# Kernel tuning notes

Measured on AMD Instinct MI355X. Metric: run time of the kernel, lower is better.

The kernel has to match this reference:

```python
import jax, jax.numpy as jnp
import numpy as np

NQ = 4            # num_qubits
DIM = 2 ** NQ     # 16-dim complex state

def _rx(theta):
    c = jnp.cos(theta / 2.0); s = jnp.sin(theta / 2.0)
    return jnp.array([[c, -1j * s], [-1j * s, c]], dtype=jnp.complex64)

def _ry(theta):
    c = jnp.cos(theta / 2.0); s = jnp.sin(theta / 2.0)
    return jnp.array([[c, -s], [s, c]], dtype=jnp.complex64)

def _apply_1q(state, q, U):
    # state: [B, 16] complex; apply 2x2 unitary U on qubit q (qubit 0 = MSB)
    B = state.shape[0]
    st = state.reshape((B,) + (2,) * NQ)
    st = jnp.moveaxis(st, 1 + q, -1)
    st = st @ U.T
    st = jnp.moveaxis(st, -1, 1 + q)
    return st.reshape(B, DIM)

def _apply_cnot(state, c, t):
    # flip target qubit t where control qubit c == 1
    B = state.shape[0]
    st = state.reshape((B,) + (2,) * NQ)
    st = jnp.moveaxis(st, (1 + c, 1 + t), (-2, -1))
    st = jnp.stack([st[..., 0, :], st[..., 1, ::-1]], axis=-2)
    st = jnp.moveaxis(st, (-2, -1), (1 + c, 1 + t))
    return st.reshape(B, DIM)

def _circuit(state):
    rx1, ry1 = _rx(0.1), _ry(0.2)
    rx2, ry2 = _rx(0.3), _ry(0.4)
    for q in range(NQ):
        state = _apply_1q(state, q, rx1)
        state = _apply_1q(state, q, ry1)
    for q in range(NQ - 1):
        state = _apply_cnot(state, q, q + 1)
    for q in range(NQ):
        state = _apply_1q(state, q, rx2)
        state = _apply_1q(state, q, ry2)
    return state

def setup_inputs() -> dict:
    key = jax.random.key(0)
    ks = jax.random.split(key, 9)
    B = 65536
    return {
        'x':   jax.random.normal(ks[0], (B, 784), dtype=jnp.float32),
        'We1': jax.random.normal(ks[1], (784, 256), dtype=jnp.float32) * 0.05,
        'be1': jnp.zeros((256,), dtype=jnp.float32),
        'We2': jax.random.normal(ks[2], (256, 32), dtype=jnp.float32) * 0.05,
        'be2': jnp.zeros((32,), dtype=jnp.float32),
        'W1':  jax.random.normal(ks[3], (32, 128), dtype=jnp.float32) * 0.05,
        'b1':  jnp.zeros((128,), dtype=jnp.float32),
        'W2':  jax.random.normal(ks[4], (128, 10), dtype=jnp.float32) * 0.05,
        'b2':  jnp.zeros((10,), dtype=jnp.float32),
    }

def reference(x, We1, be1, We2, be2, W1, b1, W2, b2):
    # encoder: Linear(784,256) -> ReLU -> Linear(256,32) -> Tanh
    h = jax.nn.relu(x @ We1 + be1)
    enc = jnp.tanh(h @ We2 + be2)               # [B, 32]
    psi = (enc[:, :DIM] + 1j * enc[:, DIM:]).astype(jnp.complex64)
    norm = jnp.sqrt(jnp.sum(jnp.abs(psi) ** 2, axis=1, keepdims=True))
    psi = psi / norm
    psi = _circuit(psi)                          # [B, 16] complex
    feat = jnp.concatenate([psi.real, psi.imag], axis=1)  # [B, 32]
    # classifier: Linear(32,128) -> ReLU -> (Dropout=identity in eval) -> Linear(128,10)
    out = jax.nn.relu(feat @ W1 + b1) @ W2 + b2
    return out
```

## Files before the change

### kernel.cpp

```cpp
#include <hip/hip_runtime.h>
#include <stdint.h>

#define DEVINL __device__ __forceinline__

typedef short bf16x8 __attribute__((ext_vector_type(8)));
typedef float f32x4  __attribute__((ext_vector_type(4)));

DEVINL uint16_t f2bf(float f) {
    uint32_t u = __builtin_bit_cast(uint32_t, f);
    uint32_t r = u + 0x7fffu + ((u >> 16) & 1u);
    return (uint16_t)(r >> 16);
}

DEVINL f32x4 mfma16x16x32(bf16x8 a, bf16x8 b, f32x4 c) {
    return __builtin_amdgcn_mfma_f32_16x16x32_bf16(a, b, c, 0, 0, 0);
}

DEVINL void async_load16(const void* g, void* l) {
    __builtin_amdgcn_global_load_lds(
        (const __attribute__((address_space(1))) void*)g,
        (__attribute__((address_space(3))) void*)l, 16, 0, 0);
}

#define WS_WE1T 0
#define WS_WE2T 425984
#define WS_W1T  442368
#define WS_W2T  450560

__global__ __launch_bounds__(256) void prep_weights(
    const float* __restrict__ We1, const float* __restrict__ We2,
    const float* __restrict__ W1,  const float* __restrict__ W2,
    uint16_t* __restrict__ We1T, uint16_t* __restrict__ We2T,
    uint16_t* __restrict__ W1T,  uint16_t* __restrict__ W2T) {
    int tid = blockIdx.x * 256 + threadIdx.x;
    if (tid < 256 * 832) {
        int n = tid / 832, k = tid % 832;
        We1T[tid] = (k < 784) ? f2bf(We1[k * 256 + n]) : (uint16_t)0;
        return;
    }
    int t2 = tid - 256 * 832;
    if (t2 < 32 * 256) {
        int n = t2 / 256, k = t2 % 256;
        We2T[t2] = f2bf(We2[k * 32 + n]);
        return;
    }
    int t3 = t2 - 32 * 256;
    if (t3 < 128 * 32) {
        int n = t3 / 32, k = t3 % 32;
        W1T[t3] = f2bf(W1[k * 128 + n]);
        return;
    }
    int t4 = t3 - 128 * 32;
    if (t4 < 16 * 128) {
        int n = t4 / 128, k = t4 % 128;
        W2T[t4] = (n < 10) ? f2bf(W2[k * 10 + n]) : (uint16_t)0;
        return;
    }
}

DEVINL void apply_rx(float* sr, float* si, int bit, float c, float s) {
    #pragma unroll
    for (int i = 0; i < 16; i++) {
        if (!(i & bit)) {
            int j = i | bit;
            float r0 = sr[i], i0 = si[i], r1 = sr[j], i1 = si[j];
            sr[i] = c * r0 + s * i1;  si[i] = c * i0 - s * r1;
            sr[j] = c * r1 + s * i0;  si[j] = c * i1 - s * r0;
        }
    }
}
DEVINL void apply_ry(float* sr, float* si, int bit, float c, float s) {
    #pragma unroll
    for (int i = 0; i < 16; i++) {
        if (!(i & bit)) {
            int j = i | bit;
            float r0 = sr[i], i0 = si[i], r1 = sr[j], i1 = si[j];
            sr[i] = c * r0 - s * r1;  si[i] = c * i0 - s * i1;
            sr[j] = s * r0 + c * r1;  si[j] = s * i0 + c * i1;
        }
    }
}
DEVINL void apply_cnot(float* sr, float* si, int cb, int tb) {
    #pragma unroll
    for (int i = 0; i < 16; i++) {
        if ((i & cb) && !(i & tb)) {
            int j = i | tb;
            float tr = sr[i]; sr[i] = sr[j]; sr[j] = tr;
            float ti = si[i]; si[i] = si[j]; si[j] = ti;
        }
    }
}
DEVINL void circuit(float* sr, float* si) {
    const float C1 = 0.99875026039496628f, S1 = 0.04997916927067833f;
    const float C2 = 0.99500416527802582f, S2 = 0.09983341664682815f;
    const float C3 = 0.98877107793604227f, S3 = 0.14943813247359922f;
    const float C4 = 0.98006657784124163f, S4 = 0.19866933079506122f;
    #pragma unroll
    for (int q = 0; q < 4; q++) {
        int bit = 8 >> q;
        apply_rx(sr, si, bit, C1, S1);
        apply_ry(sr, si, bit, C2, S2);
    }
    apply_cnot(sr, si, 8, 4);
    apply_cnot(sr, si, 4, 2);
    apply_cnot(sr, si, 2, 1);
    #pragma unroll
    for (int q = 0; q < 4; q++) {
        int bit = 8 >> q;
        apply_rx(sr, si, bit, C3, S3);
        apply_ry(sr, si, bit, C4, S4);
    }
}

__global__ __launch_bounds__(256, 4) void fused_kernel(
    const float* __restrict__ x, const uint16_t* __restrict__ We1T,
    const float* __restrict__ be1,
    const uint16_t* __restrict__ We2T, const float* __restrict__ be2,
    const uint16_t* __restrict__ W1T, const float* __restrict__ b1,
    const uint16_t* __restrict__ W2T, const float* __restrict__ b2,
    float* __restrict__ out) {
    __shared__ __align__(16) char smem[40960];
    uint16_t* Als   = (uint16_t*)smem;
    uint16_t* Bls   = (uint16_t*)(smem + 8192);
    uint16_t* Htile = (uint16_t*)smem;
    float*    encls  = (float*)smem;
    uint16_t* featls = (uint16_t*)(smem + 8448);
    uint16_t* a1ls   = (uint16_t*)(smem + 13568);

    const int t = threadIdx.x;
    const int rowbase = blockIdx.x * 64;
    const int w  = t >> 6;
    const int l  = t & 63;
    const int lm = l & 15;
    const int lq = l >> 4;

    f32x4 acc[4][4] = {};

    const int ar = t >> 2;
    const int ac = (t & 3) * 16;
    const float* xrow = x + (size_t)(rowbase + ar) * 784;
    const int aswz = ar & 7;
    const int ach0 = ((t & 3) * 2)     ^ aswz;
    const int ach1 = ((t & 3) * 2 + 1) ^ aswz;

    float4 va[4];
    #pragma unroll
    for (int j = 0; j < 4; j++) {
        int c = ac + j * 4;
        va[j] = (c < 784) ? *(const float4*)(xrow + c) : make_float4(0.f, 0.f, 0.f, 0.f);
    }

    for (int k0 = 0; k0 < 832; k0 += 64) {
        __syncthreads();

        #pragma unroll
        for (int j = 0; j < 8; j++) {
            int g  = j * 256 + t;
            int br = g >> 3;
            int bc = ((g & 7) ^ (br & 7)) * 8;
            async_load16(We1T + (size_t)br * 832 + k0 + bc, &Bls[8 * g]);
        }
        union { uint4 u4; uint16_t us[8]; } p0, p1;
        p0.us[0] = f2bf(va[0].x); p0.us[1] = f2bf(va[0].y);
        p0.us[2] = f2bf(va[0].z); p0.us[3] = f2bf(va[0].w);
        p0.us[4] = f2bf(va[1].x); p0.us[5] = f2bf(va[1].y);
        p0.us[6] = f2bf(va[1].z); p0.us[7] = f2bf(va[1].w);
        p1.us[0] = f2bf(va[2].x); p1.us[1] = f2bf(va[2].y);
        p1.us[2] = f2bf(va[2].z); p1.us[3] = f2bf(va[2].w);
        p1.us[4] = f2bf(va[3].x); p1.us[5] = f2bf(va[3].y);
        p1.us[6] = f2bf(va[3].z); p1.us[7] = f2bf(va[3].w);
        *(uint4*)&Als[ar * 64 + ach0 * 8] = p0.u4;
        *(uint4*)&Als[ar * 64 + ach1 * 8] = p1.u4;

        __syncthreads();

        {
            int kn = k0 + 64;
            if (kn < 832) {
                #pragma unroll
                for (int j = 0; j < 4; j++) {
                    int c = kn + ac + j * 4;
                    va[j] = (c < 784) ? *(const float4*)(xrow + c)
                                      : make_float4(0.f, 0.f, 0.f, 0.f);
                }
            }
        }

        #pragma unroll
        for (int kk = 0; kk < 2; kk++) {
            bf16x8 afr[4], bfr[4];
            #pragma unroll
            for (int mi = 0; mi < 4; mi++) {
                int row = mi * 16 + lm;
                int ch  = (kk * 4 + lq) ^ (lm & 7);
                afr[mi] = *(const bf16x8*)&Als[row * 64 + ch * 8];
            }
            #pragma unroll
            for (int ni = 0; ni < 4; ni++) {
                int row = w * 64 + ni * 16 + lm;
                int ch  = (kk * 4 + lq) ^ (lm & 7);
                bfr[ni] = *(const bf16x8*)&Bls[row * 64 + ch * 8];
            }
            #pragma unroll
            for (int mi = 0; mi < 4; mi++)
                #pragma unroll
                for (int ni = 0; ni < 4; ni++)
                    acc[mi][ni] = mfma16x16x32(afr[mi], bfr[ni], acc[mi][ni]);
        }
    }

    __syncthreads();

    #pragma unroll
    for (int ni = 0; ni < 4; ni++) {
        int n = w * 64 + ni * 16 + lm;
        float bias = be1[n];
        #pragma unroll
        for (int mi = 0; mi < 4; mi++) {
            #pragma unroll
            for (int i = 0; i < 4; i++) {
                int r = mi * 16 + lq * 4 + i;
                float v = acc[mi][ni][i] + bias;
                v = v > 0.f ? v : 0.f;
                Htile[r * 272 + n] = f2bf(v);
            }
        }
    }
    __syncthreads();

    f32x4 acc2[2] = {};
    #pragma unroll
    for (int k0 = 0; k0 < 256; k0 += 32) {
        bf16x8 af = *(const bf16x8*)&Htile[(w * 16 + lm) * 272 + k0 + lq * 8];
        #pragma unroll
        for (int ni = 0; ni < 2; ni++) {
            bf16x8 bf = *(const bf16x8*)&We2T[(ni * 16 + lm) * 256 + k0 + lq * 8];
            acc2[ni] = mfma16x16x32(af, bf, acc2[ni]);
        }
    }
    __syncthreads();

    #pragma unroll
    for (int ni = 0; ni < 2; ni++) {
        int col = ni * 16 + lm;
        float bias = be2[col];
        #pragma unroll
        for (int i = 0; i < 4; i++) {
            int r = w * 16 + lq * 4 + i;
            encls[r * 33 + col] = tanhf(acc2[ni][i] + bias);
        }
    }
    __syncthreads();

    if (t < 64) {
        float e[32];
        #pragma unroll
        for (int j = 0; j < 32; j++) e[j] = encls[t * 33 + j];
        float s = 0.f;
        #pragma unroll
        for (int j = 0; j < 32; j++) s += e[j] * e[j];
        float inv = 1.0f / sqrtf(s);
        float sr[16], si[16];
        #pragma unroll
        for (int i = 0; i < 16; i++) { sr[i] = e[i] * inv; si[i] = e[16 + i] * inv; }
        circuit(sr, si);
        #pragma unroll
        for (int i = 0; i < 16; i++) {
            featls[t * 40 + i]      = f2bf(sr[i]);
            featls[t * 40 + 16 + i] = f2bf(si[i]);
        }
    }
    __syncthreads();

    f32x4 acc3[8] = {};
    {
        bf16x8 af = *(const bf16x8*)&featls[(w * 16 + lm) * 40 + lq * 8];
        #pragma unroll
        for (int ni = 0; ni < 8; ni++) {
            bf16x8 bf = *(const bf16x8*)&W1T[(ni * 16 + lm) * 32 + lq * 8];
            acc3[ni] = mfma16x16x32(af, bf, acc3[ni]);
        }
    }
    #pragma unroll
    for (int ni = 0; ni < 8; ni++) {
        int col = ni * 16 + lm;
        float bias = b1[col];
        #pragma unroll
        for (int i = 0; i < 4; i++) {
            int r = w * 16 + lq * 4 + i;
            float v = acc3[ni][i] + bias;
            v = v > 0.f ? v : 0.f;
            a1ls[r * 136 + col] = f2bf(v);
        }
    }

    f32x4 acc4 = {};
    #pragma unroll
    for (int k0 = 0; k0 < 128; k0 += 32) {
        bf16x8 af = *(const bf16x8*)&a1ls[(w * 16 + lm) * 136 + k0 + lq * 8];
        bf16x8 bf = *(const bf16x8*)&W2T[lm * 128 + k0 + lq * 8];
        acc4 = mfma16x16x32(af, bf, acc4);
    }
    if (lm < 10) {
        float bias = b2[lm];
        #pragma unroll
        for (int i = 0; i < 4; i++) {
            int r = rowbase + w * 16 + lq * 4 + i;
            out[(size_t)r * 10 + lm] = acc4[i] + bias;
        }
    }
}

extern "C" void kernel_launch(void* const* d_in, const int* in_sizes, int n_in,
                              void* d_out, int out_size, void* d_ws, size_t ws_size,
                              hipStream_t stream) {
    const float* x   = (const float*)d_in[0];
    const float* We1 = (const float*)d_in[1];
    const float* be1 = (const float*)d_in[2];
    const float* We2 = (const float*)d_in[3];
    const float* be2 = (const float*)d_in[4];
    const float* W1  = (const float*)d_in[5];
    const float* b1  = (const float*)d_in[6];
    const float* W2  = (const float*)d_in[7];
    const float* b2  = (const float*)d_in[8];
    float* out = (float*)d_out;

    char* ws = (char*)d_ws;
    uint16_t* We1T = (uint16_t*)(ws + WS_WE1T);
    uint16_t* We2T = (uint16_t*)(ws + WS_WE2T);
    uint16_t* W1T  = (uint16_t*)(ws + WS_W1T);
    uint16_t* W2T  = (uint16_t*)(ws + WS_W2T);

    hipLaunchKernelGGL(prep_weights, dim3(888), dim3(256), 0, stream,
                       We1, We2, W1, W2, We1T, We2T, W1T, W2T);
    hipLaunchKernelGGL(fused_kernel, dim3(1024), dim3(256), 0, stream,
                       x, We1T, be1, We2T, be2, W1T, b1, W2T, b2, out);
}
```

Before: 333.9 us.

## Double-buffer LDS tiles in the first GEMM with a single barrier per k-step

The first-layer GEMM loop now ping-pongs between two LDS buffers. The next B tile (async global-to-LDS) and the next A tile (bf16 pack) are staged while MFMAs run on the current tile, using explicit waitcnt plus one s_barrier per iteration instead of two __syncthreads. MFMA blocks are wrapped in s_setprio, and x loads past column 784 are clamped rather than zero-filled, which relies on the padded weight columns being zero. Shared memory doubles to 80KB and launch bounds drop to 2 blocks per CU, trading occupancy for overlap.

```diff
diff --git a/kernel.cpp b/kernel.cpp
--- a/kernel.cpp
+++ b/kernel.cpp
@@ -112,16 +112,74 @@
     }
 }
 
-__global__ __launch_bounds__(256, 4) void fused_kernel(
+DEVINL void stage_B(const uint16_t* __restrict__ We1T, int k0, uint16_t* Bls, int t) {
+    #pragma unroll
+    for (int j = 0; j < 8; j++) {
+        int g  = j * 256 + t;
+        int br = g >> 3;
+        int bc = ((g & 7) ^ (br & 7)) * 8;
+        async_load16(We1T + (size_t)br * 832 + k0 + bc, &Bls[8 * g]);
+    }
+}
+
+DEVINL void pack_A(const float4* va, uint16_t* Als, int ar, int ach0, int ach1) {
+    union { uint4 u4; uint16_t us[8]; } p0, p1;
+    p0.us[0] = f2bf(va[0].x); p0.us[1] = f2bf(va[0].y);
+    p0.us[2] = f2bf(va[0].z); p0.us[3] = f2bf(va[0].w);
+    p0.us[4] = f2bf(va[1].x); p0.us[5] = f2bf(va[1].y);
+    p0.us[6] = f2bf(va[1].z); p0.us[7] = f2bf(va[1].w);
+    p1.us[0] = f2bf(va[2].x); p1.us[1] = f2bf(va[2].y);
+    p1.us[2] = f2bf(va[2].z); p1.us[3] = f2bf(va[2].w);
+    p1.us[4] = f2bf(va[3].x); p1.us[5] = f2bf(va[3].y);
+    p1.us[6] = f2bf(va[3].z); p1.us[7] = f2bf(va[3].w);
+    *(uint4*)&Als[ar * 64 + ach0 * 8] = p0.u4;
+    *(uint4*)&Als[ar * 64 + ach1 * 8] = p1.u4;
+}
+
+DEVINL void load_va(float4* va, const float* __restrict__ xrow, int k0, int ac) {
+    #pragma unroll
+    for (int j = 0; j < 4; j++) {
+        int c = k0 + ac + j * 4;
+        c = (c <= 780) ? c : 780;
+        va[j] = *(const float4*)(xrow + c);
+    }
+}
+
+DEVINL void compute_tile(const uint16_t* Als, const uint16_t* Bls,
+                         f32x4 (&acc)[4][4], int w, int lm, int lq) {
+    #pragma unroll
+    for (int kk = 0; kk < 2; kk++) {
+        bf16x8 afr[4], bfr[4];
+        #pragma unroll
+        for (int mi = 0; mi < 4; mi++) {
+            int row = mi * 16 + lm;
+            int ch  = (kk * 4 + lq) ^ (lm & 7);
+            afr[mi] = *(const bf16x8*)&Als[row * 64 + ch * 8];
+        }
+        #pragma unroll
+        for (int ni = 0; ni < 4; ni++) {
+            int row = w * 64 + ni * 16 + lm;
+            int ch  = (kk * 4 + lq) ^ (lm & 7);
+            bfr[ni] = *(const bf16x8*)&Bls[row * 64 + ch * 8];
+        }
+        __builtin_amdgcn_s_setprio(1);
+        #pragma unroll
+        for (int mi = 0; mi < 4; mi++)
+            #pragma unroll
+            for (int ni = 0; ni < 4; ni++)
+                acc[mi][ni] = mfma16x16x32(afr[mi], bfr[ni], acc[mi][ni]);
+        __builtin_amdgcn_s_setprio(0);
+    }
+}
+
+__global__ __launch_bounds__(256, 2) void fused_kernel(
     const float* __restrict__ x, const uint16_t* __restrict__ We1T,
     const float* __restrict__ be1,
     const uint16_t* __restrict__ We2T, const float* __restrict__ be2,
     const uint16_t* __restrict__ W1T, const float* __restrict__ b1,
     const uint16_t* __restrict__ W2T, const float* __restrict__ b2,
     float* __restrict__ out) {
-    __shared__ __align__(16) char smem[40960];
-    uint16_t* Als   = (uint16_t*)smem;
-    uint16_t* Bls   = (uint16_t*)(smem + 8192);
+    __shared__ __align__(16) char smem[81920];
     uint16_t* Htile = (uint16_t*)smem;
     float*    encls  = (float*)smem;
     uint16_t* featls = (uint16_t*)(smem + 8448);
@@ -139,74 +197,39 @@
     const int ar = t >> 2;
     const int ac = (t & 3) * 16;
     const float* xrow = x + (size_t)(rowbase + ar) * 784;
-    const int aswz = ar & 7;
-    const int ach0 = ((t & 3) * 2)     ^ aswz;
-    const int ach1 = ((t & 3) * 2 + 1) ^ aswz;
+    const int ach0 = ((t & 3) * 2)     ^ (ar & 7);
+    const int ach1 = ((t & 3) * 2 + 1) ^ (ar & 7);
 
     float4 va[4];
-    #pragma unroll
-    for (int j = 0; j < 4; j++) {
-        int c = ac + j * 4;
-        va[j] = (c < 784) ? *(const float4*)(xrow + c) : make_float4(0.f, 0.f, 0.f, 0.f);
-    }
-
-    for (int k0 = 0; k0 < 832; k0 += 64) {
-        __syncthreads();
-
-        #pragma unroll
-        for (int j = 0; j < 8; j++) {
-            int g  = j * 256 + t;
-            int br = g >> 3;
-            int bc = ((g & 7) ^ (br & 7)) * 8;
-            async_load16(We1T + (size_t)br * 832 + k0 + bc, &Bls[8 * g]);
-        }
-        union { uint4 u4; uint16_t us[8]; } p0, p1;
-        p0.us[0] = f2bf(va[0].x); p0.us[1] = f2bf(va[0].y);
-        p0.us[2] = f2bf(va[0].z); p0.us[3] = f2bf(va[0].w);
-        p0.us[4] = f2bf(va[1].x); p0.us[5] = f2bf(va[1].y);
-        p0.us[6] = f2bf(va[1].z); p0.us[7] = f2bf(va[1].w);
-        p1.us[0] = f2bf(va[2].x); p1.us[1] = f2bf(va[2].y);
-        p1.us[2] = f2bf(va[2].z); p1.us[3] = f2bf(va[2].w);
-        p1.us[4] = f2bf(va[3].x); p1.us[5] = f2bf(va[3].y);
-        p1.us[6] = f2bf(va[3].z); p1.us[7] = f2bf(va[3].w);
-        *(uint4*)&Als[ar * 64 + ach0 * 8] = p0.u4;
-        *(uint4*)&Als[ar * 64 + ach1 * 8] = p1.u4;
-
-        __syncthreads();
-
-        {
-            int kn = k0 + 64;
-            if (kn < 832) {
-                #pragma unroll
-                for (int j = 0; j < 4; j++) {
-                    int c = kn + ac + j * 4;
-                    va[j] = (c < 784) ? *(const float4*)(xrow + c)
-                                      : make_float4(0.f, 0.f, 0.f, 0.f);
-                }
-            }
-        }
-
-        #pragma unroll
-        for (int kk = 0; kk < 2; kk++) {
-            bf16x8 afr[4], bfr[4];
-            #pragma unroll
-            for (int mi = 0; mi < 4; mi++) {
-                int row = mi * 16 + lm;
-                int ch  = (kk * 4 + lq) ^ (lm & 7);
-                afr[mi] = *(const bf16x8*)&Als[row * 64 + ch * 8];
-            }
-            #pragma unroll
-            for (int ni = 0; ni < 4; ni++) {
-                int row = w * 64 + ni * 16 + lm;
-                int ch  = (kk * 4 + lq) ^ (lm & 7);
-                bfr[ni] = *(const bf16x8*)&Bls[row * 64 + ch * 8];
-            }
-            #pragma unroll
-            for (int mi = 0; mi < 4; mi++)
-                #pragma unroll
-                for (int ni = 0; ni < 4; ni++)
-                    acc[mi][ni] = mfma16x16x32(afr[mi], bfr[ni], acc[mi][ni]);
-        }
+
+    load_va(va, xrow, 0, ac);
+    stage_B(We1T, 0, (uint16_t*)(smem + 8192), t);
+    __builtin_amdgcn_sched_barrier(0);
+    pack_A(va, (uint16_t*)smem, ar, ach0, ach1);
+    load_va(va, xrow, 64, ac);
+    asm volatile("s_waitcnt lgkmcnt(0)" ::: "memory");
+    asm volatile("s_waitcnt vmcnt(4)" ::: "memory");
+    __builtin_amdgcn_s_barrier();
+    asm volatile("" ::: "memory");
+
+    int cur = 0;
+    for (int it = 0; it < 12; ++it) {
+        char* bc = smem + cur * 40960;
+        char* bn = smem + (cur ^ 1) * 40960;
+        stage_B(We1T, (it + 1) * 64, (uint16_t*)(bn + 8192), t);
+        __builtin_amdgcn_sched_barrier(0);
+        pack_A(va, (uint16_t*)bn, ar, ach0, ach1);
+        load_va(va, xrow, (it + 2) * 64, ac);
+        compute_tile((const uint16_t*)bc, (const uint16_t*)(bc + 8192), acc, w, lm, lq);
+        asm volatile("s_waitcnt lgkmcnt(0)" ::: "memory");
+        asm volatile("s_waitcnt vmcnt(4)" ::: "memory");
+        __builtin_amdgcn_s_barrier();
+        asm volatile("" ::: "memory");
+        cur ^= 1;
+    }
+    {
+        char* bc = smem + cur * 40960;
+        compute_tile((const uint16_t*)bc, (const uint16_t*)(bc + 8192), acc, w, lm, lq);
     }
 
     __syncthreads();
```

After: 324.7 us. 1.03x faster.
